# Kernel optimization log

Hardware: AMD Instinct MI355X
Metric: run time of the kernel (lower is better)

Reference implementation:

```python
import jax, jax.numpy as jnp
import numpy as np

N = 50000      # nodes
E = 800000     # edges (avg degree 16)
D = 256        # d_model
H = 8          # heads
C = D // H     # per-head channels = 32
DE = 64        # edge feature dim
NEG_SLOPE = 0.2
EPS = 1e-5


def setup_inputs() -> dict:
    key = jax.random.key(0)
    ks = jax.random.split(key, 12)
    s = 0.05
    return {
        "x": jax.random.normal(ks[0], (N, D), jnp.float32),
        "edge_attr": jax.random.normal(ks[1], (E, DE), jnp.float32),
        "edge_index": jax.random.randint(ks[2], (2, E), 0, N, dtype=jnp.int32),
        # GATv2Conv params (torch Linear layout: [out, in])
        "W_l": jax.random.normal(ks[3], (H * C, D), jnp.float32) * s,   # lin_l (source)
        "b_l": jnp.zeros((H * C,), jnp.float32),
        "W_r": jax.random.normal(ks[4], (H * C, D), jnp.float32) * s,   # lin_r (target)
        "b_r": jnp.zeros((H * C,), jnp.float32),
        "W_e": jax.random.normal(ks[5], (H * C, DE), jnp.float32) * s,  # lin_edge (no bias)
        "att": jax.random.normal(ks[6], (H, C), jnp.float32) * s,       # attention vector a
        "W_res": jax.random.normal(ks[7], (H * C, D), jnp.float32) * s, # residual Linear (no bias)
        "bias": jnp.zeros((H * C,), jnp.float32),                        # conv output bias
        "gamma": jnp.ones((D,), jnp.float32),                            # LayerNorm weight
        "beta": jnp.zeros((D,), jnp.float32),                            # LayerNorm bias
    }


def reference(x, edge_attr, W_l, b_l, W_r, b_r, W_e, att, W_res, bias, gamma, beta, edge_index):
    src = edge_index[0]  # j (messages flow source -> target)
    dst = edge_index[1]  # i

    xl = (x @ W_l.T + b_l).reshape(N, H, C)   # source transform
    xr = (x @ W_r.T + b_r).reshape(N, H, C)   # target transform
    ee = (edge_attr @ W_e.T).reshape(E, H, C)  # edge embedding

    # GATv2 attention logits per edge/head
    g = jax.nn.leaky_relu(xl[src] + xr[dst] + ee, NEG_SLOPE)  # [E, H, C]
    alpha = jnp.einsum("ehc,hc->eh", g, att)                   # [E, H]

    # segment softmax over incoming edges of each target node
    amax = jax.ops.segment_max(alpha, dst, num_segments=N)     # [N, H] (-inf for empty)
    ealpha = jnp.exp(alpha - amax[dst])
    denom = jax.ops.segment_sum(ealpha, dst, num_segments=N)   # [N, H]
    alpha = ealpha / jnp.where(denom > 0, denom, 1.0)[dst]

    # weighted message aggregation (scatter-add)
    msg = xl[src] * alpha[:, :, None]                          # [E, H, C]
    out = jax.ops.segment_sum(msg, dst, num_segments=N)        # [N, H, C]

    out = out.reshape(N, H * C) + x @ W_res.T + bias           # concat heads + residual + bias

    # LayerNorm over last dim
    mu = out.mean(-1, keepdims=True)
    var = ((out - mu) ** 2).mean(-1, keepdims=True)
    return (out - mu) * jax.lax.rsqrt(var + EPS) * gamma + beta
```

## Files before the change

### kernel.cpp

```cpp
#include <hip/hip_runtime.h>

#define N_NODES 50000
#define N_EDGES 800000
#define D_MODEL 256
#define H_HEADS 8
#define C_CH 32
#define DE_DIM 64
#define NEG_SLOPE 0.2f
#define LN_EPS 1e-5f
#define TILES (N_EDGES / 64)

typedef float  f32x4  __attribute__((ext_vector_type(4)));
typedef short  bf16x8 __attribute__((ext_vector_type(8)));

static __device__ __forceinline__ unsigned short f2bf(float f) {
    unsigned int u = __float_as_uint(f);
    u += 0x7fffu + ((u >> 16) & 1u);
    return (unsigned short)(u >> 16);
}
static __device__ __forceinline__ float bf2f(unsigned short s) {
    return __uint_as_float(((unsigned int)s) << 16);
}
static __device__ __forceinline__ bf16x8 load_cvt8(const float* __restrict__ p) {
    float4 a = *(const float4*)p;
    float4 b = *(const float4*)(p + 4);
    bf16x8 r;
    r[0] = (short)f2bf(a.x); r[1] = (short)f2bf(a.y);
    r[2] = (short)f2bf(a.z); r[3] = (short)f2bf(a.w);
    r[4] = (short)f2bf(b.x); r[5] = (short)f2bf(b.y);
    r[6] = (short)f2bf(b.z); r[7] = (short)f2bf(b.w);
    return r;
}

__global__ __launch_bounds__(256) void cvt_bf16_kernel(const float* __restrict__ in,
                                                       unsigned short* __restrict__ out,
                                                       int n8) {
    int g = blockIdx.x * 256 + threadIdx.x;
    if (g < n8) {
        bf16x8 v = load_cvt8(in + (size_t)g * 8);
        *(bf16x8*)(out + (size_t)g * 8) = v;
    }
}

__global__ __launch_bounds__(256) void node_gemm(const unsigned short* __restrict__ xbf,
                                                 const unsigned short* __restrict__ Wbf,
                                                 const float* __restrict__ bl,
                                                 const float* __restrict__ br,
                                                 unsigned short* __restrict__ xl,
                                                 unsigned short* __restrict__ xr,
                                                 float* __restrict__ res) {
    int tid = threadIdx.x;
    int lane = tid & 63, wv = tid >> 6;
    int quad = lane >> 4, l15 = lane & 15;
    int rowTile = blockIdx.x * 64;
    int which = blockIdx.y;
    const unsigned short* W = Wbf + (size_t)which * 65536;
    int colBase = wv * 64;

    f32x4 acc[4][4];
#pragma unroll
    for (int r = 0; r < 4; r++)
#pragma unroll
        for (int c = 0; c < 4; c++) acc[r][c] = (f32x4){0.f, 0.f, 0.f, 0.f};

#pragma unroll 1
    for (int k8 = 0; k8 < 8; ++k8) {
        int kb = k8 * 32 + quad * 8;
        bf16x8 af[4], bfr[4];
#pragma unroll
        for (int r = 0; r < 4; r++) {
            int row = rowTile + r * 16 + l15;
            if (row > N_NODES - 1) row = N_NODES - 1;
            af[r] = *(const bf16x8*)(xbf + (size_t)row * D_MODEL + kb);
        }
#pragma unroll
        for (int c = 0; c < 4; c++) {
            int col = colBase + c * 16 + l15;
            bfr[c] = *(const bf16x8*)(W + (size_t)col * D_MODEL + kb);
        }
#pragma unroll
        for (int r = 0; r < 4; r++)
#pragma unroll
            for (int c = 0; c < 4; c++)
                acc[r][c] = __builtin_amdgcn_mfma_f32_16x16x32_bf16(af[r], bfr[c], acc[r][c], 0, 0, 0);
    }

    float bv[4];
#pragma unroll
    for (int c = 0; c < 4; c++) {
        int col = colBase + c * 16 + l15;
        bv[c] = (which == 0) ? bl[col] : (which == 1 ? br[col] : 0.f);
    }
#pragma unroll
    for (int r = 0; r < 4; r++) {
#pragma unroll
        for (int g = 0; g < 4; g++) {
            int row = rowTile + r * 16 + quad * 4 + g;
            if (row < N_NODES) {
#pragma unroll
                for (int c = 0; c < 4; c++) {
                    int col = colBase + c * 16 + l15;
                    float v = acc[r][c][g] + bv[c];
                    size_t idx = (size_t)row * D_MODEL + col;
                    if (which == 0)      xl[idx] = f2bf(v);
                    else if (which == 1) xr[idx] = f2bf(v);
                    else                 res[idx] = v;
                }
            }
        }
    }
}

__global__ __launch_bounds__(256) void edge_logits(const float* __restrict__ edge_attr,
                                                   const float* __restrict__ We,
                                                   const float* __restrict__ att,
                                                   const int* __restrict__ srcP,
                                                   const int* __restrict__ dstP,
                                                   const int* __restrict__ eP,
                                                   const unsigned short* __restrict__ xl,
                                                   const unsigned short* __restrict__ xr,
                                                   float* __restrict__ alphaP) {
    __shared__ short weS[2048 * 8];

    int tid = threadIdx.x;
    int lane = tid & 63, wv = tid >> 6;
    int quad = lane >> 4, l15 = lane & 15;

    for (int g = tid; g < 2048; g += 256) {
        int c = g >> 7, kq = (g >> 6) & 1, ln = g & 63;
        int o = c * 16 + (ln & 15);
        int k = kq * 32 + (ln >> 4) * 8;
        bf16x8 v = load_cvt8(We + o * DE_DIM + k);
        *(bf16x8*)&weS[g * 8] = v;
    }
    __syncthreads();

    float attv[16];
#pragma unroll
    for (int c = 0; c < 16; c++) attv[c] = att[c * 16 + l15];

    for (int tile = blockIdx.x; tile < TILES; tile += gridDim.x) {
        int p0 = tile * 64 + wv * 16;

        int ef = eP[p0 + l15];
        bf16x8 a0 = load_cvt8(edge_attr + (size_t)ef * DE_DIM + quad * 8);
        bf16x8 a1 = load_cvt8(edge_attr + (size_t)ef * DE_DIM + 32 + quad * 8);

        int srcv[4], dstv[4];
#pragma unroll
        for (int r = 0; r < 4; r++) {
            int p = p0 + quad * 4 + r;
            srcv[r] = srcP[p];
            dstv[r] = dstP[p];
        }

        float pa[4][8];
#pragma unroll
        for (int r = 0; r < 4; r++)
#pragma unroll
            for (int h = 0; h < 8; h++) pa[r][h] = 0.f;

#pragma unroll
        for (int c = 0; c < 16; c++) {
            bf16x8 b0 = *(bf16x8*)&weS[((c * 2 + 0) * 64 + lane) * 8];
            bf16x8 b1 = *(bf16x8*)&weS[((c * 2 + 1) * 64 + lane) * 8];
            f32x4 ee = (f32x4){0.f, 0.f, 0.f, 0.f};
            ee = __builtin_amdgcn_mfma_f32_16x16x32_bf16(a0, b0, ee, 0, 0, 0);
            ee = __builtin_amdgcn_mfma_f32_16x16x32_bf16(a1, b1, ee, 0, 0, 0);
            int col = c * 16 + l15;
            float attvc = attv[c];
#pragma unroll
            for (int r = 0; r < 4; r++) {
                float xlv = bf2f(xl[(size_t)srcv[r] * D_MODEL + col]);
                float xrv = bf2f(xr[(size_t)dstv[r] * D_MODEL + col]);
                float t = ee[r] + xlv + xrv;
                t = (t > 0.f) ? t : NEG_SLOPE * t;
                pa[r][c >> 1] += t * attvc;
            }
        }
#pragma unroll
        for (int r = 0; r < 4; r++)
#pragma unroll
            for (int h = 0; h < 8; h++) {
                float v = pa[r][h];
                v += __shfl_xor(v, 1);
                v += __shfl_xor(v, 2);
                v += __shfl_xor(v, 4);
                v += __shfl_xor(v, 8);
                pa[r][h] = v;
            }
        if (l15 == 0) {
#pragma unroll
            for (int r = 0; r < 4; r++) {
                size_t pos = (size_t)(p0 + quad * 4 + r);
                *(float4*)(alphaP + pos * 8)     = make_float4(pa[r][0], pa[r][1], pa[r][2], pa[r][3]);
                *(float4*)(alphaP + pos * 8 + 4) = make_float4(pa[r][4], pa[r][5], pa[r][6], pa[r][7]);
            }
        }
    }
}

__global__ __launch_bounds__(256) void hist_kernel(const int* __restrict__ dstIdx,
                                                   int* __restrict__ cnt) {
    int e = blockIdx.x * 256 + threadIdx.x;
    if (e < N_EDGES) atomicAdd(&cnt[dstIdx[e]], 1);
}

__global__ __launch_bounds__(1024) void scan_kernel(const int* __restrict__ cnt,
                                                    int* __restrict__ off,
                                                    int* __restrict__ woff) {
    const int CHUNK = 49;
    int tid = threadIdx.x;
    int base = tid * CHUNK;
    int local[CHUNK];
    int sum = 0;
#pragma unroll
    for (int j = 0; j < CHUNK; ++j) {
        int idx = base + j;
        int v = (idx < N_NODES) ? cnt[idx] : 0;
        local[j] = sum;
        sum += v;
    }
    int lane = tid & 63, wv = tid >> 6;
    int s = sum;
#pragma unroll
    for (int ofs = 1; ofs < 64; ofs <<= 1) {
        int t2 = __shfl_up(s, ofs);
        if (lane >= ofs) s += t2;
    }
    __shared__ int wsum[16];
    __shared__ int woffS[16];
    if (lane == 63) wsum[wv] = s;
    __syncthreads();
    if (tid == 0) {
        int a = 0;
#pragma unroll
        for (int i = 0; i < 16; ++i) { woffS[i] = a; a += wsum[i]; }
    }
    __syncthreads();
    int excl = woffS[wv] + (s - sum);
#pragma unroll
    for (int j = 0; j < CHUNK; ++j) {
        int idx = base + j;
        if (idx < N_NODES) {
            int v = excl + local[j];
            off[idx] = v;
            woff[idx] = v;
        }
    }
    if (tid == 0) off[N_NODES] = N_EDGES;
}

__global__ __launch_bounds__(256) void scatter_kernel(const int* __restrict__ srcIdx,
                                                      const int* __restrict__ dstIdx,
                                                      int* __restrict__ woff,
                                                      int* __restrict__ srcP,
                                                      int* __restrict__ dstP,
                                                      int* __restrict__ eP) {
    int e = blockIdx.x * 256 + threadIdx.x;
    if (e < N_EDGES) {
        int d = dstIdx[e];
        int pos = atomicAdd(&woff[d], 1);
        srcP[pos] = srcIdx[e];
        dstP[pos] = d;
        eP[pos]   = e;
    }
}

__global__ __launch_bounds__(256) void aggregate_ln(const int* __restrict__ off,
                                                    const int* __restrict__ srcP,
                                                    const float* __restrict__ alphaP,
                                                    const unsigned short* __restrict__ xl,
                                                    const float* __restrict__ res,
                                                    const float* __restrict__ biasc,
                                                    const float* __restrict__ gamma,
                                                    const float* __restrict__ beta,
                                                    float* __restrict__ out) {
    int wv = threadIdx.x >> 6, lane = threadIdx.x & 63;
    int i = blockIdx.x * 4 + wv;
    int beg = off[i], end = off[i + 1];
    int h = lane >> 3;

    float acc0 = 0.f, acc1 = 0.f, acc2 = 0.f, acc3 = 0.f, s = 0.f;

    int p = beg;
    int src_n = 0; float a_n = 0.f;
    if (p < end) {
        src_n = srcP[p];
        a_n   = alphaP[(size_t)p * 8 + h];
    }
    while (p < end) {
        int src = src_n; float a = a_n;
        int pn = p + 1;
        if (pn < end) {
            src_n = srcP[pn];
            a_n   = alphaP[(size_t)pn * 8 + h];
        }
        ushort4 v = *(const ushort4*)(xl + (size_t)src * D_MODEL + lane * 4);
        float w = __expf(a);
        s += w;
        acc0 = fmaf(w, bf2f(v.x), acc0);
        acc1 = fmaf(w, bf2f(v.y), acc1);
        acc2 = fmaf(w, bf2f(v.z), acc2);
        acc3 = fmaf(w, bf2f(v.w), acc3);
        p = pn;
    }

    float rs = (end > beg) ? (1.f / s) : 0.f;
    float4 r4 = *(const float4*)(res + (size_t)i * D_MODEL + lane * 4);
    float4 b4 = *(const float4*)(biasc + lane * 4);
    float v0 = acc0 * rs + r4.x + b4.x;
    float v1 = acc1 * rs + r4.y + b4.y;
    float v2 = acc2 * rs + r4.z + b4.z;
    float v3 = acc3 * rs + r4.w + b4.w;

    float sum = v0 + v1 + v2 + v3;
    float sq  = v0 * v0 + v1 * v1 + v2 * v2 + v3 * v3;
#pragma unroll
    for (int msk = 32; msk >= 1; msk >>= 1) {
        sum += __shfl_xor(sum, msk);
        sq  += __shfl_xor(sq, msk);
    }
    float mu  = sum * (1.f / 256.f);
    float var = sq * (1.f / 256.f) - mu * mu;
    var = fmaxf(var, 0.f);
    float inv = rsqrtf(var + LN_EPS);

    float4 g4 = *(const float4*)(gamma + lane * 4);
    float4 be4 = *(const float4*)(beta + lane * 4);
    float4 o4;
    o4.x = (v0 - mu) * inv * g4.x + be4.x;
    o4.y = (v1 - mu) * inv * g4.y + be4.y;
    o4.z = (v2 - mu) * inv * g4.z + be4.z;
    o4.w = (v3 - mu) * inv * g4.w + be4.w;
    *(float4*)(out + (size_t)i * D_MODEL + lane * 4) = o4;
}

extern "C" void kernel_launch(void* const* d_in, const int* in_sizes, int n_in,
                              void* d_out, int out_size, void* d_ws, size_t ws_size,
                              hipStream_t stream) {
    const float* x         = (const float*)d_in[0];
    const float* edge_attr = (const float*)d_in[1];
    const int*   edge_index= (const int*)d_in[2];
    const float* Wl        = (const float*)d_in[3];
    const float* bl        = (const float*)d_in[4];
    const float* Wr        = (const float*)d_in[5];
    const float* br        = (const float*)d_in[6];
    const float* We        = (const float*)d_in[7];
    const float* att       = (const float*)d_in[8];
    const float* Wres      = (const float*)d_in[9];
    const float* biasc     = (const float*)d_in[10];
    const float* gamma     = (const float*)d_in[11];
    const float* beta      = (const float*)d_in[12];
    const int* srcIdx = edge_index;
    const int* dstIdx = edge_index + N_EDGES;
    float* out = (float*)d_out;

    char* ws = (char*)d_ws;
    unsigned short* xl  = (unsigned short*)ws;
    unsigned short* xr  = xl + (size_t)N_NODES * D_MODEL;
    unsigned short* xbf = xr + (size_t)N_NODES * D_MODEL;
    unsigned short* Wbf = xbf + (size_t)N_NODES * D_MODEL;
    float* res    = (float*)(Wbf + 3 * 65536);
    float* alphaP = res + (size_t)N_NODES * D_MODEL;
    int* cnt   = (int*)(alphaP + (size_t)N_EDGES * 8);
    int* off   = cnt + N_NODES;
    int* woff  = off + (N_NODES + 1);
    int* srcP  = woff + N_NODES;
    int* dstP  = srcP + N_EDGES;
    int* eP    = dstP + N_EDGES;
    (void)ws_size; (void)n_in; (void)in_sizes; (void)out_size;

    hipMemsetAsync(cnt, 0, N_NODES * sizeof(int), stream);

    cvt_bf16_kernel<<<(N_NODES * D_MODEL / 8 + 255) / 256, 256, 0, stream>>>(x, xbf, N_NODES * D_MODEL / 8);
    cvt_bf16_kernel<<<32, 256, 0, stream>>>(Wl,   Wbf,             65536 / 8);
    cvt_bf16_kernel<<<32, 256, 0, stream>>>(Wr,   Wbf + 65536,     65536 / 8);
    cvt_bf16_kernel<<<32, 256, 0, stream>>>(Wres, Wbf + 2 * 65536, 65536 / 8);

    dim3 g1((N_NODES + 63) / 64, 3);
    node_gemm<<<g1, 256, 0, stream>>>(xbf, Wbf, bl, br, xl, xr, res);

    hist_kernel<<<(N_EDGES + 255) / 256, 256, 0, stream>>>(dstIdx, cnt);
    scan_kernel<<<1, 1024, 0, stream>>>(cnt, off, woff);
    scatter_kernel<<<(N_EDGES + 255) / 256, 256, 0, stream>>>(srcIdx, dstIdx, woff, srcP, dstP, eP);

    edge_logits<<<1024, 256, 0, stream>>>(edge_attr, We, att, srcP, dstP, eP, xl, xr, alphaP);

    aggregate_ln<<<N_NODES / 4, 256, 0, stream>>>(off, srcP, alphaP, xl, res,
                                                  biasc, gamma, beta, out);
}
```

Before: 1.035 ms.

## Process edges in original order in edge_logits and scatter logits via position map

edge_logits now walks edges in their original order, so edge_attr rows are read contiguously instead of gathered through a permutation. Each logit is written to its CSR-sorted slot through a new posOf array that scatter_kernel records, and the dstP and eP arrays are dropped. The att vector moves into shared memory, the kernel gets launch bounds for higher occupancy, and the grid grows from 1024 to 2500 blocks. The cost is that alpha writes become scattered, and xr gathers by destination lose the locality that sorted order gave them.

Measured after the change: 1.253 ms. 21.1% more time.

```diff
diff --git a/kernel.cpp b/kernel.cpp
--- a/kernel.cpp
+++ b/kernel.cpp
@@ -111,16 +111,17 @@
     }
 }
 
-__global__ __launch_bounds__(256) void edge_logits(const float* __restrict__ edge_attr,
-                                                   const float* __restrict__ We,
-                                                   const float* __restrict__ att,
-                                                   const int* __restrict__ srcP,
-                                                   const int* __restrict__ dstP,
-                                                   const int* __restrict__ eP,
-                                                   const unsigned short* __restrict__ xl,
-                                                   const unsigned short* __restrict__ xr,
-                                                   float* __restrict__ alphaP) {
+__global__ __launch_bounds__(256, 4) void edge_logits(const float* __restrict__ edge_attr,
+                                                      const float* __restrict__ We,
+                                                      const float* __restrict__ att,
+                                                      const int* __restrict__ srcIdx,
+                                                      const int* __restrict__ dstIdx,
+                                                      const int* __restrict__ posOf,
+                                                      const unsigned short* __restrict__ xl,
+                                                      const unsigned short* __restrict__ xr,
+                                                      float* __restrict__ alphaP) {
     __shared__ short weS[2048 * 8];
+    __shared__ float attS[256];
 
     int tid = threadIdx.x;
     int lane = tid & 63, wv = tid >> 6;
@@ -133,25 +134,23 @@
         bf16x8 v = load_cvt8(We + o * DE_DIM + k);
         *(bf16x8*)&weS[g * 8] = v;
     }
+    if (tid < 256) attS[tid] = att[tid];
     __syncthreads();
 
-    float attv[16];
-#pragma unroll
-    for (int c = 0; c < 16; c++) attv[c] = att[c * 16 + l15];
-
     for (int tile = blockIdx.x; tile < TILES; tile += gridDim.x) {
-        int p0 = tile * 64 + wv * 16;
-
-        int ef = eP[p0 + l15];
-        bf16x8 a0 = load_cvt8(edge_attr + (size_t)ef * DE_DIM + quad * 8);
-        bf16x8 a1 = load_cvt8(edge_attr + (size_t)ef * DE_DIM + 32 + quad * 8);
-
-        int srcv[4], dstv[4];
+        int e0 = tile * 64 + wv * 16;
+
+        int eA = e0 + l15;
+        bf16x8 a0 = load_cvt8(edge_attr + (size_t)eA * DE_DIM + quad * 8);
+        bf16x8 a1 = load_cvt8(edge_attr + (size_t)eA * DE_DIM + 32 + quad * 8);
+
+        int srcv[4], dstv[4], posv[4];
 #pragma unroll
         for (int r = 0; r < 4; r++) {
-            int p = p0 + quad * 4 + r;
-            srcv[r] = srcP[p];
-            dstv[r] = dstP[p];
+            int e = e0 + quad * 4 + r;
+            srcv[r] = srcIdx[e];
+            dstv[r] = dstIdx[e];
+            posv[r] = posOf[e];
         }
 
         float pa[4][8];
@@ -168,7 +167,7 @@
             ee = __builtin_amdgcn_mfma_f32_16x16x32_bf16(a0, b0, ee, 0, 0, 0);
             ee = __builtin_amdgcn_mfma_f32_16x16x32_bf16(a1, b1, ee, 0, 0, 0);
             int col = c * 16 + l15;
-            float attvc = attv[c];
+            float attvc = attS[col];
 #pragma unroll
             for (int r = 0; r < 4; r++) {
                 float xlv = bf2f(xl[(size_t)srcv[r] * D_MODEL + col]);
@@ -192,7 +191,7 @@
         if (l15 == 0) {
 #pragma unroll
             for (int r = 0; r < 4; r++) {
-                size_t pos = (size_t)(p0 + quad * 4 + r);
+                size_t pos = (size_t)posv[r];
                 *(float4*)(alphaP + pos * 8)     = make_float4(pa[r][0], pa[r][1], pa[r][2], pa[r][3]);
                 *(float4*)(alphaP + pos * 8 + 4) = make_float4(pa[r][4], pa[r][5], pa[r][6], pa[r][7]);
             }
@@ -254,16 +253,13 @@
 __global__ __launch_bounds__(256) void scatter_kernel(const int* __restrict__ srcIdx,
                                                       const int* __restrict__ dstIdx,
                                                       int* __restrict__ woff,
-                                                      int* __restrict__ srcP,
-                                                      int* __restrict__ dstP,
-                                                      int* __restrict__ eP) {
+                                                      int* __restrict__ posOf,
+                                                      int* __restrict__ srcP) {
     int e = blockIdx.x * 256 + threadIdx.x;
     if (e < N_EDGES) {
-        int d = dstIdx[e];
-        int pos = atomicAdd(&woff[d], 1);
+        int pos = atomicAdd(&woff[dstIdx[e]], 1);
+        posOf[e] = pos;
         srcP[pos] = srcIdx[e];
-        dstP[pos] = d;
-        eP[pos]   = e;
     }
 }
 
@@ -366,9 +362,8 @@
     int* cnt   = (int*)(alphaP + (size_t)N_EDGES * 8);
     int* off   = cnt + N_NODES;
     int* woff  = off + (N_NODES + 1);
-    int* srcP  = woff + N_NODES;
-    int* dstP  = srcP + N_EDGES;
-    int* eP    = dstP + N_EDGES;
+    int* posOf = woff + N_NODES;
+    int* srcP  = posOf + N_EDGES;
     (void)ws_size; (void)n_in; (void)in_sizes; (void)out_size;
 
     hipMemsetAsync(cnt, 0, N_NODES * sizeof(int), stream);
@@ -383,9 +378,9 @@
 
     hist_kernel<<<(N_EDGES + 255) / 256, 256, 0, stream>>>(dstIdx, cnt);
     scan_kernel<<<1, 1024, 0, stream>>>(cnt, off, woff);
-    scatter_kernel<<<(N_EDGES + 255) / 256, 256, 0, stream>>>(srcIdx, dstIdx, woff, srcP, dstP, eP);
-
-    edge_logits<<<1024, 256, 0, stream>>>(edge_attr, We, att, srcP, dstP, eP, xl, xr, alphaP);
+    scatter_kernel<<<(N_EDGES + 255) / 256, 256, 0, stream>>>(srcIdx, dstIdx, woff, posOf, srcP);
+
+    edge_logits<<<2500, 256, 0, stream>>>(edge_attr, We, att, srcIdx, dstIdx, posOf, xl, xr, alphaP);
 
     aggregate_ln<<<N_NODES / 4, 256, 0, stream>>>(off, srcP, alphaP, xl, res,
                                                   biasc, gamma, beta, out);
```
